# Kernel optimization log

Measured on AMD Instinct MI355X. Metric: run time of the kernel, lower is better.

Reference implementation:

```python
import jax, jax.numpy as jnp
import numpy as np

N = 50000           # nodes
E = 1_600_000       # edges (avg degree 32)
DIN_N = 128         # in_dim_n
DIN_E = 64          # in_dim_e
DOUT_N = 64         # out_dim_n
DOUT_E = 64         # out_dim_e
SLOPE = 0.01        # torch F.leaky_relu default negative_slope


def _lrelu(x):
    return jnp.where(x >= 0, x, SLOPE * x)


def setup_inputs() -> dict:
    key = jax.random.key(0)
    ks = jax.random.split(key, 8)
    nfeats = jax.random.normal(ks[0], (N, DIN_N), dtype=jnp.float32)
    efeats = jax.random.normal(ks[1], (E, DIN_E), dtype=jnp.float32)
    src = jax.random.randint(ks[2], (E,), 0, N)
    dst = jax.random.randint(ks[3], (E,), 0, N)
    # learned params (xavier-ish scaling)
    W_fc = jax.random.normal(ks[4], (DOUT_N, DIN_N), dtype=jnp.float32) / np.sqrt(DIN_N)
    d_cat = DIN_E + 2 * DOUT_N
    W_edge = jax.random.normal(ks[5], (DOUT_E, d_cat), dtype=jnp.float32) / np.sqrt(d_cat)
    b_edge = jnp.zeros((DOUT_E,), dtype=jnp.float32)
    w_coef = jax.random.normal(ks[6], (1, DOUT_E), dtype=jnp.float32) / np.sqrt(DOUT_E)
    return {"nfeats": nfeats, "efeats": efeats, "src": src, "dst": dst,
            "W_fc": W_fc, "W_edge": W_edge, "b_edge": b_edge, "w_coef": w_coef}


def reference(nfeats, efeats, src, dst, W_fc, W_edge, b_edge, w_coef):
    # node projection: z = fc(nfeats)  (bias=False)
    z = nfeats @ W_fc.T                                   # [N, DOUT_N]
    # per-edge: concat(src_z, edge_feats, dst_z) -> linear -> leaky_relu
    stacked = jnp.concatenate([z[src], efeats, z[dst]], axis=1)   # [E, DIN_E+2*DOUT_N]
    feat = _lrelu(stacked @ W_edge.T + b_edge)            # [E, DOUT_E]
    # attention logit: linear -> leaky_relu applied twice (as in source)
    a = _lrelu(_lrelu(feat @ w_coef.T))                   # [E, 1]
    # segment softmax over incoming edges of each dst node
    m = jax.lax.stop_gradient(jax.ops.segment_max(a, dst, num_segments=N))  # [N,1]
    ex = jnp.exp(a - m[dst])                              # [E, 1]
    denom = jax.ops.segment_sum(ex, dst, num_segments=N)  # [N, 1]
    alpha = ex / denom[dst]                               # [E, 1]
    # weighted aggregation of src projections back to dst nodes
    h = jax.ops.segment_sum(alpha * z[src], dst, num_segments=N)  # [N, DOUT_N]
    return (h, feat)
```

## Files before the change

kernel.cpp:

```cpp
#include <hip/hip_runtime.h>
#include <hip/hip_bf16.h>


typedef __attribute__((ext_vector_type(8))) short short8;
typedef __attribute__((ext_vector_type(4))) float f32x4;
typedef __attribute__((ext_vector_type(2))) int i32x2;

__device__ __forceinline__ short bf1(float f) {
    union { __hip_bfloat16 h; short s; } u;
    u.h = __float2bfloat16(f);
    return u.s;
}

__device__ __forceinline__ float bf2f(unsigned short u) {
    union { unsigned v; float f; } w; w.v = ((unsigned)u) << 16; return w.f;
}

__device__ __forceinline__ short8 pack8(f32x4 a, f32x4 b) {
    short8 r;
    r[0] = bf1(a[0]); r[1] = bf1(a[1]); r[2] = bf1(a[2]); r[3] = bf1(a[3]);
    r[4] = bf1(b[0]); r[5] = bf1(b[1]); r[6] = bf1(b[2]); r[7] = bf1(b[3]);
    return r;
}

__device__ __forceinline__ f32x4 ntld4(const float* p) {
    return __builtin_nontemporal_load((const f32x4*)p);
}

__device__ __forceinline__ f32x4 ld4(const float* p) {
    return *(const f32x4*)p;
}

#define MFMA16(A, B, C) __builtin_amdgcn_mfma_f32_16x16x32_bf16((A), (B), (C), 0, 0, 0)

__global__ __launch_bounds__(256) void k0_wpq(
    const float* __restrict__ W_edge, const float* __restrict__ W_fc,
    unsigned short* __restrict__ wp_bf, unsigned short* __restrict__ wq_bf)
{
    const int i = blockIdx.x * 256 + threadIdx.x;
    if (i >= 64 * 128) return;
    const int c = i >> 7, k = i & 127;
    float sp = 0.f, sq = 0.f;
    for (int j = 0; j < 64; ++j) {
        const float f = W_fc[j * 128 + k];
        sp += W_edge[c * 192 + j] * f;
        sq += W_edge[c * 192 + 128 + j] * f;
    }
    wp_bf[i] = (unsigned short)bf1(sp);
    wq_bf[i] = (unsigned short)bf1(sq);
}

__global__ __launch_bounds__(256) void k12_node(
    const float* __restrict__ nfeats, const float* __restrict__ W_fc,
    const unsigned short* __restrict__ wp_bf, const unsigned short* __restrict__ wq_bf,
    const float* __restrict__ b_edge,
    unsigned short* __restrict__ z_bf, unsigned short* __restrict__ p_bf,
    unsigned short* __restrict__ q_bf, int* __restrict__ deg, int ntiles)
{
    const int lane = threadIdx.x & 63;
    const int wave = threadIdx.x >> 6;
    const int l15 = lane & 15, g = lane >> 4;
    const int ti = blockIdx.x * 4 + wave;
    if (ti >= ntiles) return;
    const int n0 = ti * 16;

    if (lane < 16) deg[n0 + lane] = 0;

    const float* xp = nfeats + (long)(n0 + l15) * 128 + g * 8;
    short8 Ax[4];
#pragma unroll
    for (int kt = 0; kt < 4; ++kt)
        Ax[kt] = pack8(ntld4(xp + kt * 32), ntld4(xp + kt * 32 + 4));

#pragma unroll
    for (int t = 0; t < 4; ++t) {
        const int col = t * 16 + l15;
        f32x4 az = (f32x4){0.f, 0.f, 0.f, 0.f};
        f32x4 ap = az, aq = az;
#pragma unroll
        for (int kt = 0; kt < 4; ++kt) {
            const float* bz = W_fc + (long)col * 128 + kt * 32 + g * 8;
            az = MFMA16(Ax[kt], pack8(ld4(bz), ld4(bz + 4)), az);
            const short8 bp = *(const short8*)(wp_bf + (long)col * 128 + kt * 32 + g * 8);
            ap = MFMA16(Ax[kt], bp, ap);
            const short8 bq = *(const short8*)(wq_bf + (long)col * 128 + kt * 32 + g * 8);
            aq = MFMA16(Ax[kt], bq, aq);
        }
        const float bias = b_edge[col];
#pragma unroll
        for (int r = 0; r < 4; ++r) {
            const long row = n0 + g * 4 + r;
            z_bf[row * 64 + col] = (unsigned short)bf1(az[r]);
            p_bf[row * 64 + col] = (unsigned short)bf1(ap[r] + bias);
            q_bf[row * 64 + col] = (unsigned short)bf1(aq[r]);
        }
    }
}

#define LOAD_PQ(T, PQ) {                                                    \
    const int sE_ = __shfl(sAll, (T) * 16 + l15, 64);                       \
    const int dE_ = __shfl(dAll, (T) * 16 + l15, 64);                       \
    const unsigned short* pp_ = p_bf + (long)sE_ * 64 + g * 8;              \
    PQ[0] = *(const short8*)pp_;                                            \
    PQ[1] = *(const short8*)(pp_ + 32);                                     \
    const unsigned short* qp_ = q_bf + (long)dE_ * 64 + g * 8;              \
    PQ[2] = *(const short8*)qp_;                                            \
    PQ[3] = *(const short8*)(qp_ + 32);                                     \
}

#define STAGE_EF(T) {                                                       \
    const float* gs_ = efeats + (wbase + (T) * 16) * 64;                    \
    _Pragma("unroll")                                                       \
    for (int i_ = 0; i_ < 4; ++i_) {                                        \
        const int L_ = i_ * 64 + lane;                                      \
        const int G_ = (L_ & ~15) | ((L_ & 15) ^ ((L_ >> 4) & 7));          \
        __builtin_amdgcn_global_load_lds(                                   \
            (const __attribute__((address_space(1))) unsigned int*)(gs_ + G_ * 4), \
            (__attribute__((address_space(3))) unsigned int*)(&efb[wave][i_ * 256]), \
            16, 0, 0);                                                      \
    }                                                                       \
}

#define EF_READ(E0, E1, E2, E3) {                                           \
    const float* eb2_ = &efb[wave][0];                                      \
    const int ro_ = l15 * 64, sx_ = l15 & 7;                                \
    E0 = *(const f32x4*)(eb2_ + ro_ + (((2 * g    ) ^ sx_) << 2));          \
    E1 = *(const f32x4*)(eb2_ + ro_ + (((2 * g + 1) ^ sx_) << 2));          \
    E2 = *(const f32x4*)(eb2_ + ro_ + (((2 * g + 8) ^ sx_) << 2));          \
    E3 = *(const f32x4*)(eb2_ + ro_ + (((2 * g + 9) ^ sx_) << 2));          \
}

#define VMW asm volatile("s_waitcnt vmcnt(16)" ::: "memory");

#define DO_TILE(T, PQ, DOWAIT, DOPQ, DOSTAGE) {                             \
    const long eb_ = wbase + (T) * 16;                                      \
    DOWAIT                                                                  \
    f32x4 e0_, e1_, e2_, e3_;                                               \
    EF_READ(e0_, e1_, e2_, e3_);                                            \
    DOPQ                                                                    \
    asm volatile("s_waitcnt lgkmcnt(0)" ::: "memory");                      \
    DOSTAGE                                                                 \
    f32x4 acc_[4];                                                          \
    _Pragma("unroll")                                                       \
    for (int t = 0; t < 4; ++t) acc_[t] = (f32x4){0.f, 0.f, 0.f, 0.f};      \
    acc_[0] = MFMA16(PQ[0], IdA, acc_[0]);                                  \
    acc_[1] = MFMA16(PQ[0], IdB, acc_[1]);                                  \
    acc_[2] = MFMA16(PQ[1], IdA, acc_[2]);                                  \
    acc_[3] = MFMA16(PQ[1], IdB, acc_[3]);                                  \
    acc_[0] = MFMA16(PQ[2], IdA, acc_[0]);                                  \
    acc_[1] = MFMA16(PQ[2], IdB, acc_[1]);                                  \
    acc_[2] = MFMA16(PQ[3], IdA, acc_[2]);                                  \
    acc_[3] = MFMA16(PQ[3], IdB, acc_[3]);                                  \
    short8 Aef0_ = pack8(e0_, e1_), Aef1_ = pack8(e2_, e3_);                \
    _Pragma("unroll")                                                       \
    for (int t = 0; t < 4; ++t) {                                           \
        acc_[t] = MFMA16(Aef0_, W2f[t * 64 + lane], acc_[t]);               \
        acc_[t] = MFMA16(Aef1_, W2f[(4 + t) * 64 + lane], acc_[t]);         \
    }                                                                       \
    float myex_ = 0.f;                                                      \
    _Pragma("unroll")                                                       \
    for (int r = 0; r < 4; ++r) {                                           \
        float s_ = 0.f;                                                     \
        _Pragma("unroll")                                                   \
        for (int t = 0; t < 4; ++t) {                                       \
            float v_ = acc_[t][r];                                          \
            v_ = (v_ >= 0.f) ? v_ : 0.01f * v_;                             \
            __builtin_nontemporal_store(v_,                                 \
                feat_out + (eb_ + g * 4 + r) * 64 + t * 16 + l15);          \
            s_ += v_ * wc[t];                                               \
        }                                                                   \
        s_ += __shfl_xor(s_, 1, 16);                                        \
        s_ += __shfl_xor(s_, 2, 16);                                        \
        s_ += __shfl_xor(s_, 4, 16);                                        \
        s_ += __shfl_xor(s_, 8, 16);                                        \
        s_ = (s_ >= 0.f) ? s_ : 0.01f * s_;                                 \
        s_ = (s_ >= 0.f) ? s_ : 0.01f * s_;                                 \
        const float ex_ = __expf(s_);                                       \
        if (l15 == r) myex_ = ex_;                                          \
    }                                                                       \
    const int dmine_ = __shfl(dAll, (T) * 16 + g * 4 + (l15 & 3), 64);      \
    if (l15 < 4) {                                                          \
        exbuf[eb_ + g * 4 + l15] = myex_;                                   \
        rank[eb_ + g * 4 + l15] = atomicAdd(&deg[dmine_], 1);               \
    }                                                                       \
}

__global__ __launch_bounds__(512, 4) void k3_edges(
    const float* __restrict__ efeats, const int* __restrict__ src,
    const int* __restrict__ dst, const float* __restrict__ W_edge,
    const float* __restrict__ w_coef, const unsigned short* __restrict__ p_bf,
    const unsigned short* __restrict__ q_bf, float* __restrict__ feat_out,
    float* __restrict__ exbuf, int* __restrict__ deg, int* __restrict__ rank)
{
    __shared__ short8 W2f[512];
    __shared__ float efb[8][1024];

    const int tid = threadIdx.x;
    const int lane = tid & 63;
    const int wave = tid >> 6;
    const int l15 = lane & 15, g = lane >> 4;
    const long wbase = ((long)blockIdx.x * 8 + wave) * 64;

    STAGE_EF(0);
    const int sAll = src[wbase + lane];
    const int dAll = dst[wbase + lane];

    {
        const int fi = tid;
        const int s = fi >> 6, l = fi & 63;
        const int col = (s & 3) * 16 + (l & 15);
        const int gg = l >> 4, kt = s >> 2;
        const float* wp = W_edge + col * 192 + 64 + kt * 32 + gg * 8;
        W2f[fi] = pack8(ld4(wp), ld4(wp + 4));
    }

    float wc[4];
#pragma unroll
    for (int t = 0; t < 4; ++t) wc[t] = w_coef[t * 16 + l15];

    const short one = (short)0x3F80;
    short8 IdA, IdB;
#pragma unroll
    for (int jj = 0; jj < 8; ++jj) {
        IdA[jj] = (l15 == g * 8 + jj) ? one : (short)0;
        IdB[jj] = (16 + l15 == g * 8 + jj) ? one : (short)0;
    }

    short8 pqA[4], pqB[4];
    LOAD_PQ(0, pqA);
    __syncthreads();

    DO_TILE(0, pqA, ,    { LOAD_PQ(1, pqB); }, { STAGE_EF(1); });
    DO_TILE(1, pqB, VMW, { LOAD_PQ(2, pqA); }, { STAGE_EF(2); });
    DO_TILE(2, pqA, VMW, { LOAD_PQ(3, pqB); }, { STAGE_EF(3); });
    DO_TILE(3, pqB, VMW, , );
}

__global__ __launch_bounds__(256) void k_scan1(
    const int* __restrict__ deg, int* __restrict__ bsum, int N)
{
    __shared__ int ws4[4];
    const int tid = threadIdx.x, lane = tid & 63, wave = tid >> 6;
    const int i0 = blockIdx.x * 1024 + tid * 4;
    int s = 0;
#pragma unroll
    for (int jj = 0; jj < 4; ++jj) {
        const int i = i0 + jj;
        if (i < N) s += deg[i];
    }
#pragma unroll
    for (int d = 1; d < 64; d <<= 1) s += __shfl_xor(s, d, 64);
    if (lane == 0) ws4[wave] = s;
    __syncthreads();
    if (tid == 0) bsum[blockIdx.x] = ws4[0] + ws4[1] + ws4[2] + ws4[3];
}

__global__ __launch_bounds__(64) void k_scan2(
    const int* __restrict__ bsum, int* __restrict__ bpre,
    int* __restrict__ off, int nb, int N)
{
    const int t = threadIdx.x;
    const int v = (t < nb) ? bsum[t] : 0;
    int x = v;
#pragma unroll
    for (int d = 1; d < 64; d <<= 1) {
        int y = __shfl_up(x, d, 64);
        if (t >= d) x += y;
    }
    if (t < nb) bpre[t] = x - v;
    if (t == 63) off[N] = x;
}

__global__ __launch_bounds__(256) void k_scan3(
    const int* __restrict__ deg, const int* __restrict__ bpre,
    int* __restrict__ off, int N)
{
    __shared__ int ws4[4];
    const int tid = threadIdx.x, lane = tid & 63, wave = tid >> 6;
    const int i0 = blockIdx.x * 1024 + tid * 4;
    int v[4];
#pragma unroll
    for (int jj = 0; jj < 4; ++jj) {
        const int i = i0 + jj;
        v[jj] = (i < N) ? deg[i] : 0;
    }
    const int s = v[0] + v[1] + v[2] + v[3];
    int x = s;
#pragma unroll
    for (int d = 1; d < 64; d <<= 1) {
        int y = __shfl_up(x, d, 64);
        if (lane >= d) x += y;
    }
    if (lane == 63) ws4[wave] = x;
    __syncthreads();
    int wpre = 0;
#pragma unroll
    for (int w = 0; w < 4; ++w) if (w < wave) wpre += ws4[w];
    int run = bpre[blockIdx.x] + wpre + (x - s);
#pragma unroll
    for (int jj = 0; jj < 4; ++jj) {
        const int i = i0 + jj;
        if (i < N) off[i] = run;
        run += v[jj];
    }
}

__global__ __launch_bounds__(256) void k_scatter(
    const int* __restrict__ src, const int* __restrict__ dst,
    const float* __restrict__ exbuf, const int* __restrict__ off,
    const int* __restrict__ rank, i32x2* __restrict__ pairs, long E)
{
    const long e = (long)blockIdx.x * 256 + threadIdx.x;
    if (e >= E) return;
    const int d = dst[e];
    const int pos = off[d] + rank[e];
    i32x2 pr;
    pr[0] = src[e];
    pr[1] = __float_as_int(exbuf[e]);
    pairs[pos] = pr;
}

__global__ __launch_bounds__(256) void k5_aggregate(
    const int* __restrict__ off, const i32x2* __restrict__ pairs,
    const unsigned short* __restrict__ z_bf, float* __restrict__ h, int N)
{
    const int wave = threadIdx.x >> 6, lane = threadIdx.x & 63;
    const int n = blockIdx.x * 4 + wave;
    if (n >= N) return;
    const int beg = off[n], end = off[n + 1];
    float den = 0.f;
    float a0 = 0.f, a1 = 0.f, a2 = 0.f, a3 = 0.f;
    for (int base = beg; base < end; base += 64) {
        const int rem = end - base;
        i32x2 pr = (i32x2){0, 0};
        if (lane < rem) pr = __builtin_nontemporal_load(&pairs[base + lane]);
        const float ex = __int_as_float(pr[1]);
        float t = ex;
#pragma unroll
        for (int d = 1; d < 64; d <<= 1) t += __shfl_xor(t, d, 64);
        den += t;
        const int cnt = rem < 64 ? rem : 64;
        const int cnt4 = (cnt + 3) & ~3;
        for (int j = 0; j < cnt4; j += 4) {
            const int s0 = __shfl(pr[0], j, 64);
            const int s1 = __shfl(pr[0], j + 1, 64);
            const int s2 = __shfl(pr[0], j + 2, 64);
            const int s3 = __shfl(pr[0], j + 3, 64);
            const float e0 = __shfl(ex, j, 64);
            const float e1 = __shfl(ex, j + 1, 64);
            const float e2 = __shfl(ex, j + 2, 64);
            const float e3 = __shfl(ex, j + 3, 64);
            a0 = fmaf(e0, bf2f(z_bf[(long)s0 * 64 + lane]), a0);
            a1 = fmaf(e1, bf2f(z_bf[(long)s1 * 64 + lane]), a1);
            a2 = fmaf(e2, bf2f(z_bf[(long)s2 * 64 + lane]), a2);
            a3 = fmaf(e3, bf2f(z_bf[(long)s3 * 64 + lane]), a3);
        }
    }
    const float acc = (a0 + a1) + (a2 + a3);
    __builtin_nontemporal_store((end > beg) ? acc / den : 0.f,
                                h + (long)n * 64 + lane);
}

extern "C" void kernel_launch(void* const* d_in, const int* in_sizes, int n_in,
                              void* d_out, int out_size, void* d_ws, size_t ws_size,
                              hipStream_t stream) {
    const float* nfeats = (const float*)d_in[0];
    const float* efeats = (const float*)d_in[1];
    const int*   src    = (const int*)d_in[2];
    const int*   dst    = (const int*)d_in[3];
    const float* W_fc   = (const float*)d_in[4];
    const float* W_edge = (const float*)d_in[5];
    const float* b_edge = (const float*)d_in[6];
    const float* w_coef = (const float*)d_in[7];

    const int  N = in_sizes[0] / 128;
    const long E = in_sizes[2];
    const int  nb = (N + 1023) / 1024;
    const int  ntiles = N / 16;

    float* h    = (float*)d_out;
    float* feat = (float*)d_out + (long)N * 64;

    unsigned short* z_bf   = (unsigned short*)d_ws;
    unsigned short* p_bf   = z_bf + (long)N * 64;
    unsigned short* q_bf   = p_bf + (long)N * 64;
    unsigned short* wp_bf  = q_bf + (long)N * 64;
    unsigned short* wq_bf  = wp_bf + 64 * 128;
    float*          exbuf  = (float*)(wq_bf + 64 * 128);
    int*            deg    = (int*)(exbuf + E);
    int*            rank   = deg + N;
    int*            off    = rank + E;
    i32x2*          pairs  = (i32x2*)(off + N + 2);
    int*            bsum   = (int*)(pairs + E);
    int*            bpre   = bsum + 64;

    k0_wpq<<<32, 256, 0, stream>>>(W_edge, W_fc, wp_bf, wq_bf);
    k12_node<<<(ntiles + 3) / 4, 256, 0, stream>>>(nfeats, W_fc, wp_bf, wq_bf,
                                                   b_edge, z_bf, p_bf, q_bf,
                                                   deg, ntiles);
    k3_edges<<<(int)(E / 512), 512, 0, stream>>>(efeats, src, dst, W_edge, w_coef,
                                                 p_bf, q_bf, feat, exbuf, deg, rank);
    k_scan1<<<nb, 256, 0, stream>>>(deg, bsum, N);
    k_scan2<<<1, 64, 0, stream>>>(bsum, bpre, off, nb, N);
    k_scan3<<<nb, 256, 0, stream>>>(deg, bpre, off, N);
    k_scatter<<<(int)((E + 255) / 256), 256, 0, stream>>>(src, dst, exbuf, off,
                                                          rank, pairs, E);
    k5_aggregate<<<(N + 3) / 4, 256, 0, stream>>>(off, pairs, z_bf, h, N);
}
```

Measured before the change: 339.5 us.

## Build CSR offsets before edge kernel and scatter pairs directly from it

Degree counting and rank assignment move into a separate small atomic kernel that runs first, and the prefix scan follows it. The edge kernel can then write (src, exp) pairs straight into CSR position, so the separate scatter kernel and the exbuf round trip are removed. This trades an extra pass over dst, plus a memset, for dropping one full pass over E elements and the exbuf write and read. The edge kernel now does a dependent off/rank gather and a random 8-byte store per edge.

```diff
diff --git a/kernel.cpp b/kernel.cpp
--- a/kernel.cpp
+++ b/kernel.cpp
@@ -32,6 +32,15 @@
 }
 
 #define MFMA16(A, B, C) __builtin_amdgcn_mfma_f32_16x16x32_bf16((A), (B), (C), 0, 0, 0)
+
+__global__ __launch_bounds__(256) void k_deg(
+    const int* __restrict__ dst, int* __restrict__ deg,
+    int* __restrict__ rank, long E)
+{
+    const long e = (long)blockIdx.x * 256 + threadIdx.x;
+    if (e >= E) return;
+    rank[e] = atomicAdd(&deg[dst[e]], 1);
+}
 
 __global__ __launch_bounds__(256) void k0_wpq(
     const float* __restrict__ W_edge, const float* __restrict__ W_fc,
@@ -55,7 +64,7 @@
     const unsigned short* __restrict__ wp_bf, const unsigned short* __restrict__ wq_bf,
     const float* __restrict__ b_edge,
     unsigned short* __restrict__ z_bf, unsigned short* __restrict__ p_bf,
-    unsigned short* __restrict__ q_bf, int* __restrict__ deg, int ntiles)
+    unsigned short* __restrict__ q_bf, int ntiles)
 {
     const int lane = threadIdx.x & 63;
     const int wave = threadIdx.x >> 6;
@@ -63,8 +72,6 @@
     const int ti = blockIdx.x * 4 + wave;
     if (ti >= ntiles) return;
     const int n0 = ti * 16;
-
-    if (lane < 16) deg[n0 + lane] = 0;
 
     const float* xp = nfeats + (long)(n0 + l15) * 128 + g * 8;
     short8 Ax[4];
@@ -179,9 +186,14 @@
         if (l15 == r) myex_ = ex_;                                          \
     }                                                                       \
     const int dmine_ = __shfl(dAll, (T) * 16 + g * 4 + (l15 & 3), 64);      \
+    const int smine_ = __shfl(sAll, (T) * 16 + g * 4 + (l15 & 3), 64);      \
     if (l15 < 4) {                                                          \
-        exbuf[eb_ + g * 4 + l15] = myex_;                                   \
-        rank[eb_ + g * 4 + l15] = atomicAdd(&deg[dmine_], 1);               \
+        const long e_ = eb_ + g * 4 + l15;                                  \
+        const int pos_ = off[dmine_] + rank[e_];                            \
+        i32x2 pr_;                                                          \
+        pr_[0] = smine_;                                                    \
+        pr_[1] = __float_as_int(myex_);                                     \
+        pairs[pos_] = pr_;                                                  \
     }                                                                       \
 }
 
@@ -190,7 +202,8 @@
     const int* __restrict__ dst, const float* __restrict__ W_edge,
     const float* __restrict__ w_coef, const unsigned short* __restrict__ p_bf,
     const unsigned short* __restrict__ q_bf, float* __restrict__ feat_out,
-    float* __restrict__ exbuf, int* __restrict__ deg, int* __restrict__ rank)
+    const int* __restrict__ off, const int* __restrict__ rank,
+    i32x2* __restrict__ pairs)
 {
     __shared__ short8 W2f[512];
     __shared__ float efb[8][1024];
@@ -303,21 +316,6 @@
         if (i < N) off[i] = run;
         run += v[jj];
     }
-}
-
-__global__ __launch_bounds__(256) void k_scatter(
-    const int* __restrict__ src, const int* __restrict__ dst,
-    const float* __restrict__ exbuf, const int* __restrict__ off,
-    const int* __restrict__ rank, i32x2* __restrict__ pairs, long E)
-{
-    const long e = (long)blockIdx.x * 256 + threadIdx.x;
-    if (e >= E) return;
-    const int d = dst[e];
-    const int pos = off[d] + rank[e];
-    i32x2 pr;
-    pr[0] = src[e];
-    pr[1] = __float_as_int(exbuf[e]);
-    pairs[pos] = pr;
 }
 
 __global__ __launch_bounds__(256) void k5_aggregate(
@@ -386,24 +384,23 @@
     unsigned short* q_bf   = p_bf + (long)N * 64;
     unsigned short* wp_bf  = q_bf + (long)N * 64;
     unsigned short* wq_bf  = wp_bf + 64 * 128;
-    float*          exbuf  = (float*)(wq_bf + 64 * 128);
-    int*            deg    = (int*)(exbuf + E);
+    int*            deg    = (int*)(wq_bf + 64 * 128);
     int*            rank   = deg + N;
     int*            off    = rank + E;
     i32x2*          pairs  = (i32x2*)(off + N + 2);
     int*            bsum   = (int*)(pairs + E);
     int*            bpre   = bsum + 64;
 
-    k0_wpq<<<32, 256, 0, stream>>>(W_edge, W_fc, wp_bf, wq_bf);
-    k12_node<<<(ntiles + 3) / 4, 256, 0, stream>>>(nfeats, W_fc, wp_bf, wq_bf,
-                                                   b_edge, z_bf, p_bf, q_bf,
-                                                   deg, ntiles);
-    k3_edges<<<(int)(E / 512), 512, 0, stream>>>(efeats, src, dst, W_edge, w_coef,
-                                                 p_bf, q_bf, feat, exbuf, deg, rank);
+    (void)hipMemsetAsync(deg, 0, (size_t)N * sizeof(int), stream);
+
+    k_deg<<<(int)((E + 255) / 256), 256, 0, stream>>>(dst, deg, rank, E);
     k_scan1<<<nb, 256, 0, stream>>>(deg, bsum, N);
     k_scan2<<<1, 64, 0, stream>>>(bsum, bpre, off, nb, N);
     k_scan3<<<nb, 256, 0, stream>>>(deg, bpre, off, N);
-    k_scatter<<<(int)((E + 255) / 256), 256, 0, stream>>>(src, dst, exbuf, off,
-                                                          rank, pairs, E);
+    k0_wpq<<<32, 256, 0, stream>>>(W_edge, W_fc, wp_bf, wq_bf);
+    k12_node<<<(ntiles + 3) / 4, 256, 0, stream>>>(nfeats, W_fc, wp_bf, wq_bf,
+                                                   b_edge, z_bf, p_bf, q_bf, ntiles);
+    k3_edges<<<(int)(E / 512), 512, 0, stream>>>(efeats, src, dst, W_edge, w_coef,
+                                                 p_bf, q_bf, feat, off, rank, pairs);
     k5_aggregate<<<(N + 3) / 4, 256, 0, stream>>>(off, pairs, z_bf, h, N);
 }
```

New measurement: 400.7 us. +18.0%, slower.
